# Optimization experiments

Hardware: AMD Instinct MI355X
Metric: run time of the kernel (lower is better)

The kernel has to match this reference:

```python
import jax, jax.numpy as jnp
import numpy as np

B, N, E = 32, 128, 8192
IMG, LOC, H = 2048, 5, 128


def setup_inputs() -> dict:
    key = jax.random.key(0)
    ks = jax.random.split(key, 10)
    img_feat = jax.random.normal(ks[0], (B, N, IMG), dtype=jnp.float32)
    img_loc = jax.random.uniform(ks[1], (B, N, LOC), dtype=jnp.float32)
    edge_src = jax.random.randint(ks[2], (E,), 0, N, dtype=jnp.int32)
    edge_dst = jax.random.randint(ks[3], (E,), 0, N, dtype=jnp.int32)
    # learned parameters (nn.Linear: y = x @ W + b)
    W_img = jax.random.normal(ks[4], (IMG, H), dtype=jnp.float32) / np.sqrt(IMG)
    b_img = jnp.zeros((H,), dtype=jnp.float32)
    W_loc = jax.random.normal(ks[5], (LOC, H), dtype=jnp.float32) / np.sqrt(LOC)
    b_loc = jnp.zeros((H,), dtype=jnp.float32)
    W_rel = jax.random.normal(ks[6], (2 * H, H), dtype=jnp.float32) / np.sqrt(2 * H)
    b_rel = jnp.zeros((H,), dtype=jnp.float32)
    return {
        "img_feat": img_feat, "img_loc": img_loc,
        "edge_src": edge_src, "edge_dst": edge_dst,
        "W_img": W_img, "b_img": b_img,
        "W_loc": W_loc, "b_loc": b_loc,
        "W_rel": W_rel, "b_rel": b_rel,
    }


def reference(img_feat, img_loc, edge_src, edge_dst,
              W_img, b_img, W_loc, b_loc, W_rel, b_rel):
    # img_fc / img_loc_fc projections
    img = jnp.einsum('bni,ih->bnh', img_feat, W_img) + b_img      # [B,N,H]
    loc = jnp.einsum('bnl,lh->bnh', img_loc, W_loc) + b_loc       # [B,N,H]
    node_feat = img + loc                                          # [B,N,H]
    # per-edge gather + concat + linear (batched over all edges at once;
    # split W_rel to avoid materializing the concat)
    src_f = jnp.take(img, edge_src, axis=1)                        # [B,E,H]
    dst_f = jnp.take(img, edge_dst, axis=1)                        # [B,E,H]
    edge_feat = (jnp.einsum('beh,hk->bek', src_f, W_rel[:H]) +
                 jnp.einsum('beh,hk->bek', dst_f, W_rel[H:]) + b_rel)  # [B,E,H]
    return node_feat, edge_feat
```

## Files before the change

kernel.cpp:

```cpp
#include <hip/hip_runtime.h>
#include <hip/hip_bf16.h>
#include <stdint.h>

#define B_   32
#define N_   128
#define E_   8192
#define IMG_ 2048
#define H_   128

typedef __attribute__((ext_vector_type(8))) short bf16x8;
typedef __attribute__((ext_vector_type(4))) float f32x4;

__device__ inline uint16_t f2bf(float x) {
    uint32_t u = __float_as_uint(x);
    uint32_t r = (u + 0x7FFFu + ((u >> 16) & 1u)) >> 16;
    return (uint16_t)r;
}
__device__ inline float bf2f(short x) {
    return __uint_as_float(((uint32_t)(uint16_t)x) << 16);
}

__global__ __launch_bounds__(256) void prep_kernel(
    const float* __restrict__ W_img, const float* __restrict__ W_rel,
    uint16_t* __restrict__ Wt_img, uint16_t* __restrict__ Wt_rel) {
    int bid = blockIdx.x, tid = threadIdx.x;
    if (bid < 32) {
        __shared__ float t[64][129];
        int k0 = bid * 64;
        const float* src = W_img + (size_t)k0 * H_;
        #pragma unroll
        for (int it = 0; it < 32; it++) {
            int idx = it * 256 + tid;
            t[idx >> 7][idx & 127] = src[idx];
        }
        __syncthreads();
        int c = tid >> 1, kh = (tid & 1) * 32;
        uint16_t* dst = Wt_img + (size_t)c * IMG_ + k0 + kh;
        #pragma unroll
        for (int j = 0; j < 32; j++) dst[j] = f2bf(t[kh + j][c]);
    } else {
        int t2 = (bid - 32) * 256 + tid;
        int c = t2 >> 8, k = t2 & 255;
        Wt_rel[t2] = f2bf(W_rel[k * H_ + c]);
    }
}

__global__ __launch_bounds__(1024) void node_proj_kernel(
    const float* __restrict__ img_feat,
    const uint16_t* __restrict__ Wt_img,
    const uint16_t* __restrict__ Wt_rel,
    const float* __restrict__ img_loc,
    const float* __restrict__ b_img,
    const float* __restrict__ W_loc,
    const float* __restrict__ b_loc,
    const float* __restrict__ b_rel,
    float* __restrict__ out_node,
    uint16_t* __restrict__ proj) {
    __shared__ __align__(16) char lds_raw[131072];
    float (*red)[16][128] = (float (*)[16][128])lds_raw;
    uint16_t (*imgb)[136] = (uint16_t (*)[136])lds_raw;

    int strip = blockIdx.x;
    int tid = threadIdx.x;
    int w  = tid >> 6;
    int l  = tid & 63;
    int lr = l & 15;
    int kq = l >> 4;

    const char* gA = (const char*)(img_feat + (size_t)strip * 16 * IMG_);
    #pragma unroll
    for (int r = 0; r < 8; r++) {
        int L = r * 16384 + tid * 16;
        int row = L >> 13;
        int koff = L & 8191;
        int gsrc = row * 8192 + (koff ^ ((row & 7) << 4));
        __builtin_amdgcn_global_load_lds(
            (const __attribute__((address_space(1))) void*)(gA + gsrc),
            (__attribute__((address_space(3))) void*)(lds_raw + L), 16, 0, 0);
    }

    int kbase = w * 128 + kq * 8;
    bf16x8 bcur[8];
    #pragma unroll
    for (int n = 0; n < 8; n++)
        bcur[n] = *(const bf16x8*)(Wt_img + (size_t)(n * 16 + lr) * IMG_ + kbase);

    __syncthreads();

    f32x4 acc[8];
    #pragma unroll
    for (int n = 0; n < 8; n++) acc[n] = (f32x4){0.f, 0.f, 0.f, 0.f};
    int sw = (lr & 7) << 4;
    #pragma unroll
    for (int ks = 0; ks < 4; ks++) {
        int koffb = w * 512 + ks * 128 + kq * 32;
        float4 a0 = *(const float4*)(lds_raw + (size_t)lr * 8192 + (koffb ^ sw));
        float4 a1 = *(const float4*)(lds_raw + (size_t)lr * 8192 + ((koffb + 16) ^ sw));
        bf16x8 bn[8];
        if (ks < 3) {
            int kn = kbase + (ks + 1) * 32;
            #pragma unroll
            for (int n = 0; n < 8; n++)
                bn[n] = *(const bf16x8*)(Wt_img + (size_t)(n * 16 + lr) * IMG_ + kn);
        }
        bf16x8 af;
        af[0] = (short)f2bf(a0.x); af[1] = (short)f2bf(a0.y);
        af[2] = (short)f2bf(a0.z); af[3] = (short)f2bf(a0.w);
        af[4] = (short)f2bf(a1.x); af[5] = (short)f2bf(a1.y);
        af[6] = (short)f2bf(a1.z); af[7] = (short)f2bf(a1.w);
        #pragma unroll
        for (int n = 0; n < 8; n++)
            acc[n] = __builtin_amdgcn_mfma_f32_16x16x32_bf16(af, bcur[n], acc[n], 0, 0, 0);
        if (ks < 3) {
            #pragma unroll
            for (int n = 0; n < 8; n++) bcur[n] = bn[n];
        }
    }
    __syncthreads();

    #pragma unroll
    for (int n = 0; n < 8; n++)
        #pragma unroll
        for (int r = 0; r < 4; r++)
            red[w][kq * 4 + r][n * 16 + lr] = acc[n][r];
    __syncthreads();

    int row0 = tid >> 7, col = tid & 127;
    int row1 = row0 + 8;
    float s0 = 0.f, s1 = 0.f;
    #pragma unroll
    for (int ww = 0; ww < 16; ww++) {
        s0 += red[ww][row0][col];
        s1 += red[ww][row1][col];
    }
    __syncthreads();

    {
        float bi = b_img[col];
        float bl = b_loc[col];
        float wl[5];
        #pragma unroll
        for (int j = 0; j < 5; j++) wl[j] = W_loc[j * H_ + col];
        float img0 = s0 + bi, img1 = s1 + bi;
        int g0 = strip * 16 + row0, g1 = strip * 16 + row1;
        const float* lc0 = img_loc + g0 * 5;
        const float* lc1 = img_loc + g1 * 5;
        float loc0 = bl, loc1 = bl;
        #pragma unroll
        for (int j = 0; j < 5; j++) { loc0 += lc0[j] * wl[j]; loc1 += lc1[j] * wl[j]; }
        out_node[(size_t)g0 * H_ + col] = img0 + loc0;
        out_node[(size_t)g1 * H_ + col] = img1 + loc1;
        imgb[row0][col] = f2bf(img0);
        imgb[row1][col] = f2bf(img1);
    }
    __syncthreads();

    int kl = kq * 8;
    int cp = w * 16 + lr;
    const uint16_t* bbase = (cp < 128)
        ? (Wt_rel + (size_t)cp * 256)
        : (Wt_rel + (size_t)(cp - 128) * 256 + 128);
    f32x4 pacc = (f32x4){0.f, 0.f, 0.f, 0.f};
    #pragma unroll
    for (int ks = 0; ks < 4; ks++) {
        int k = ks * 32 + kl;
        bf16x8 af = *(const bf16x8*)(&imgb[lr][k]);
        bf16x8 bf = *(const bf16x8*)(bbase + k);
        pacc = __builtin_amdgcn_mfma_f32_16x16x32_bf16(af, bf, pacc, 0, 0, 0);
    }
    float brel = (cp < 128) ? b_rel[cp] : 0.f;
    #pragma unroll
    for (int r = 0; r < 4; r++) {
        int grow = strip * 16 + kq * 4 + r;
        proj[(size_t)grow * 256 + cp] = f2bf(pacc[r] + brel);
    }
}

__global__ __launch_bounds__(256) void edge_kernel(
    const uint16_t* __restrict__ proj,
    const int* __restrict__ edge_src,
    const int* __restrict__ edge_dst,
    float* __restrict__ out_edge) {
    int t = blockIdx.x * 256 + threadIdx.x;
    #pragma unroll
    for (int it = 0; it < 8; it++) {
        int g = t + it * 524288;
        int b = g >> 17;
        int r = g & 131071;
        int e = r >> 4;
        int c = (r & 15) * 8;
        int s = edge_src[e];
        int d = edge_dst[e];
        bf16x8 a  = *(const bf16x8*)(proj + (((size_t)b * N_ + s) * 256 + c));
        bf16x8 bb = *(const bf16x8*)(proj + (((size_t)b * N_ + d) * 256 + 128 + c));
        float* op = out_edge + ((size_t)b * E_ + e) * (size_t)H_ + c;
        float4 o0, o1;
        o0.x = bf2f(a[0]) + bf2f(bb[0]);
        o0.y = bf2f(a[1]) + bf2f(bb[1]);
        o0.z = bf2f(a[2]) + bf2f(bb[2]);
        o0.w = bf2f(a[3]) + bf2f(bb[3]);
        o1.x = bf2f(a[4]) + bf2f(bb[4]);
        o1.y = bf2f(a[5]) + bf2f(bb[5]);
        o1.z = bf2f(a[6]) + bf2f(bb[6]);
        o1.w = bf2f(a[7]) + bf2f(bb[7]);
        *(float4*)op = o0;
        *(float4*)(op + 4) = o1;
    }
}

extern "C" void kernel_launch(void* const* d_in, const int* in_sizes, int n_in,
                              void* d_out, int out_size, void* d_ws, size_t ws_size,
                              hipStream_t stream) {
    const float* img_feat = (const float*)d_in[0];
    const float* img_loc  = (const float*)d_in[1];
    const int*   edge_src = (const int*)d_in[2];
    const int*   edge_dst = (const int*)d_in[3];
    const float* W_img    = (const float*)d_in[4];
    const float* b_img    = (const float*)d_in[5];
    const float* W_loc    = (const float*)d_in[6];
    const float* b_loc    = (const float*)d_in[7];
    const float* W_rel    = (const float*)d_in[8];
    const float* b_rel    = (const float*)d_in[9];

    float* out_node = (float*)d_out;
    float* out_edge = out_node + (size_t)B_ * N_ * H_;

    char* ws = (char*)d_ws;
    uint16_t* Wt_img = (uint16_t*)ws;
    uint16_t* Wt_rel = (uint16_t*)(ws + 524288);
    uint16_t* proj   = (uint16_t*)(ws + 524288 + 65536);

    prep_kernel<<<dim3(160), dim3(256), 0, stream>>>(W_img, W_rel, Wt_img, Wt_rel);

    node_proj_kernel<<<dim3(256), dim3(1024), 0, stream>>>(
        img_feat, Wt_img, Wt_rel, img_loc, b_img, W_loc, b_loc, b_rel,
        out_node, proj);

    edge_kernel<<<dim3(2048), dim3(256), 0, stream>>>(
        proj, edge_src, edge_dst, out_edge);
}
```

Measured before the change: 58.02 us.

## Fuse prep, node projection and edge gather into one kernel with flag sync

Merges the three launches into a single persistent kernel. The last 32 blocks also transpose and convert the weights, and signal readiness through a global atomic counter that all blocks spin on. Each block publishes per-batch completion flags after writing its proj rows, then runs its share of the edge gather batch by batch, waiting on those flags, and writes with nontemporal stores. This removes launch gaps and lets edge output writes overlap with the remaining projection work. In exchange it adds a memset, spin-wait latency, and a dependence on all 256 blocks being co-resident to avoid deadlock.

```diff
diff --git a/kernel.cpp b/kernel.cpp
--- a/kernel.cpp
+++ b/kernel.cpp
@@ -20,54 +20,63 @@
     return __uint_as_float(((uint32_t)(uint16_t)x) << 16);
 }
 
-__global__ __launch_bounds__(256) void prep_kernel(
-    const float* __restrict__ W_img, const float* __restrict__ W_rel,
-    uint16_t* __restrict__ Wt_img, uint16_t* __restrict__ Wt_rel) {
-    int bid = blockIdx.x, tid = threadIdx.x;
-    if (bid < 32) {
-        __shared__ float t[64][129];
-        int k0 = bid * 64;
-        const float* src = W_img + (size_t)k0 * H_;
-        #pragma unroll
-        for (int it = 0; it < 32; it++) {
-            int idx = it * 256 + tid;
-            t[idx >> 7][idx & 127] = src[idx];
-        }
-        __syncthreads();
-        int c = tid >> 1, kh = (tid & 1) * 32;
-        uint16_t* dst = Wt_img + (size_t)c * IMG_ + k0 + kh;
-        #pragma unroll
-        for (int j = 0; j < 32; j++) dst[j] = f2bf(t[kh + j][c]);
-    } else {
-        int t2 = (bid - 32) * 256 + tid;
-        int c = t2 >> 8, k = t2 & 255;
-        Wt_rel[t2] = f2bf(W_rel[k * H_ + c]);
-    }
-}
-
-__global__ __launch_bounds__(1024) void node_proj_kernel(
+__global__ __launch_bounds__(1024) void fused_kernel(
     const float* __restrict__ img_feat,
-    const uint16_t* __restrict__ Wt_img,
-    const uint16_t* __restrict__ Wt_rel,
     const float* __restrict__ img_loc,
+    const int* __restrict__ edge_src,
+    const int* __restrict__ edge_dst,
+    const float* __restrict__ W_img,
     const float* __restrict__ b_img,
     const float* __restrict__ W_loc,
     const float* __restrict__ b_loc,
+    const float* __restrict__ W_rel,
     const float* __restrict__ b_rel,
     float* __restrict__ out_node,
-    uint16_t* __restrict__ proj) {
+    float* __restrict__ out_edge,
+    uint16_t* __restrict__ Wt_img,
+    uint16_t* __restrict__ Wt_rel,
+    uint16_t* __restrict__ proj,
+    int* flags) {
     __shared__ __align__(16) char lds_raw[131072];
     float (*red)[16][128] = (float (*)[16][128])lds_raw;
     uint16_t (*imgb)[136] = (uint16_t (*)[136])lds_raw;
-
-    int strip = blockIdx.x;
+    float (*tT)[129] = (float (*)[129])lds_raw;
+
+    int bid = blockIdx.x;
     int tid = threadIdx.x;
     int w  = tid >> 6;
     int l  = tid & 63;
     int lr = l & 15;
     int kq = l >> 4;
 
-    const char* gA = (const char*)(img_feat + (size_t)strip * 16 * IMG_);
+    if (bid >= 224) {
+        int pb = bid - 224;
+        int k0 = pb * 64;
+        const float* src = W_img + (size_t)k0 * H_;
+        #pragma unroll
+        for (int it = 0; it < 8; it++) {
+            int idx = it * 1024 + tid;
+            tT[idx >> 7][idx & 127] = src[idx];
+        }
+        __syncthreads();
+        {
+            int c = tid >> 3, kh = (tid & 7) * 8;
+            uint16_t* dst = Wt_img + (size_t)c * IMG_ + k0 + kh;
+            #pragma unroll
+            for (int j = 0; j < 8; j++) dst[j] = f2bf(tT[kh + j][c]);
+        }
+        {
+            int t2 = pb * 1024 + tid;
+            int c2 = t2 >> 8, k2 = t2 & 255;
+            Wt_rel[t2] = f2bf(W_rel[k2 * H_ + c2]);
+        }
+        __syncthreads();
+        if (tid == 0)
+            __hip_atomic_fetch_add(&flags[0], 1, __ATOMIC_RELEASE,
+                                   __HIP_MEMORY_SCOPE_AGENT);
+    }
+
+    const char* gA = (const char*)(img_feat + (size_t)bid * 16 * IMG_);
     #pragma unroll
     for (int r = 0; r < 8; r++) {
         int L = r * 16384 + tid * 16;
@@ -79,13 +88,19 @@
             (__attribute__((address_space(3))) void*)(lds_raw + L), 16, 0, 0);
     }
 
+    if (tid == 0) {
+        while (__hip_atomic_load(&flags[0], __ATOMIC_RELAXED,
+                                 __HIP_MEMORY_SCOPE_AGENT) < 32) {}
+        (void)__hip_atomic_load(&flags[0], __ATOMIC_ACQUIRE,
+                                __HIP_MEMORY_SCOPE_AGENT);
+    }
+    __syncthreads();
+
     int kbase = w * 128 + kq * 8;
     bf16x8 bcur[8];
     #pragma unroll
     for (int n = 0; n < 8; n++)
         bcur[n] = *(const bf16x8*)(Wt_img + (size_t)(n * 16 + lr) * IMG_ + kbase);
-
-    __syncthreads();
 
     f32x4 acc[8];
     #pragma unroll
@@ -142,7 +157,7 @@
         #pragma unroll
         for (int j = 0; j < 5; j++) wl[j] = W_loc[j * H_ + col];
         float img0 = s0 + bi, img1 = s1 + bi;
-        int g0 = strip * 16 + row0, g1 = strip * 16 + row1;
+        int g0 = bid * 16 + row0, g1 = bid * 16 + row1;
         const float* lc0 = img_loc + g0 * 5;
         const float* lc1 = img_loc + g1 * 5;
         float loc0 = bl, loc1 = bl;
@@ -155,56 +170,65 @@
     }
     __syncthreads();
 
-    int kl = kq * 8;
-    int cp = w * 16 + lr;
-    const uint16_t* bbase = (cp < 128)
-        ? (Wt_rel + (size_t)cp * 256)
-        : (Wt_rel + (size_t)(cp - 128) * 256 + 128);
-    f32x4 pacc = (f32x4){0.f, 0.f, 0.f, 0.f};
-    #pragma unroll
-    for (int ks = 0; ks < 4; ks++) {
-        int k = ks * 32 + kl;
-        bf16x8 af = *(const bf16x8*)(&imgb[lr][k]);
-        bf16x8 bf = *(const bf16x8*)(bbase + k);
-        pacc = __builtin_amdgcn_mfma_f32_16x16x32_bf16(af, bf, pacc, 0, 0, 0);
-    }
-    float brel = (cp < 128) ? b_rel[cp] : 0.f;
-    #pragma unroll
-    for (int r = 0; r < 4; r++) {
-        int grow = strip * 16 + kq * 4 + r;
-        proj[(size_t)grow * 256 + cp] = f2bf(pacc[r] + brel);
-    }
-}
-
-__global__ __launch_bounds__(256) void edge_kernel(
-    const uint16_t* __restrict__ proj,
-    const int* __restrict__ edge_src,
-    const int* __restrict__ edge_dst,
-    float* __restrict__ out_edge) {
-    int t = blockIdx.x * 256 + threadIdx.x;
-    #pragma unroll
-    for (int it = 0; it < 8; it++) {
-        int g = t + it * 524288;
-        int b = g >> 17;
-        int r = g & 131071;
-        int e = r >> 4;
-        int c = (r & 15) * 8;
-        int s = edge_src[e];
-        int d = edge_dst[e];
-        bf16x8 a  = *(const bf16x8*)(proj + (((size_t)b * N_ + s) * 256 + c));
-        bf16x8 bb = *(const bf16x8*)(proj + (((size_t)b * N_ + d) * 256 + 128 + c));
-        float* op = out_edge + ((size_t)b * E_ + e) * (size_t)H_ + c;
-        float4 o0, o1;
-        o0.x = bf2f(a[0]) + bf2f(bb[0]);
-        o0.y = bf2f(a[1]) + bf2f(bb[1]);
-        o0.z = bf2f(a[2]) + bf2f(bb[2]);
-        o0.w = bf2f(a[3]) + bf2f(bb[3]);
-        o1.x = bf2f(a[4]) + bf2f(bb[4]);
-        o1.y = bf2f(a[5]) + bf2f(bb[5]);
-        o1.z = bf2f(a[6]) + bf2f(bb[6]);
-        o1.w = bf2f(a[7]) + bf2f(bb[7]);
-        *(float4*)op = o0;
-        *(float4*)(op + 4) = o1;
+    {
+        int kl = kq * 8;
+        int cp = w * 16 + lr;
+        const uint16_t* bbase = (cp < 128)
+            ? (Wt_rel + (size_t)cp * 256)
+            : (Wt_rel + (size_t)(cp - 128) * 256 + 128);
+        f32x4 pacc = (f32x4){0.f, 0.f, 0.f, 0.f};
+        #pragma unroll
+        for (int ks = 0; ks < 4; ks++) {
+            int k = ks * 32 + kl;
+            bf16x8 af = *(const bf16x8*)(&imgb[lr][k]);
+            bf16x8 bf = *(const bf16x8*)(bbase + k);
+            pacc = __builtin_amdgcn_mfma_f32_16x16x32_bf16(af, bf, pacc, 0, 0, 0);
+        }
+        float brel = (cp < 128) ? b_rel[cp] : 0.f;
+        #pragma unroll
+        for (int r = 0; r < 4; r++) {
+            int grow = bid * 16 + kq * 4 + r;
+            proj[(size_t)grow * 256 + cp] = f2bf(pacc[r] + brel);
+        }
+    }
+    __syncthreads();
+    if (tid == 0)
+        __hip_atomic_fetch_add(&flags[1 + (bid >> 3)], 1, __ATOMIC_RELEASE,
+                               __HIP_MEMORY_SCOPE_AGENT);
+
+    int halfsel = tid >> 9;
+    int o = (bid << 9) | (tid & 511);
+    int e = o >> 4, c = (o & 15) << 3;
+    int s = edge_src[e], d = edge_dst[e];
+    const uint16_t* ps = proj + (size_t)s * 256 + c;
+    const uint16_t* pd = proj + (size_t)d * 256 + 128 + c;
+    float* op = out_edge + (size_t)e * H_ + c;
+
+    for (int ib = 0; ib < 16; ib++) {
+        if (tid == 0) {
+            while (__hip_atomic_load(&flags[1 + 2 * ib], __ATOMIC_RELAXED,
+                                     __HIP_MEMORY_SCOPE_AGENT) < 8 ||
+                   __hip_atomic_load(&flags[2 + 2 * ib], __ATOMIC_RELAXED,
+                                     __HIP_MEMORY_SCOPE_AGENT) < 8) {}
+            (void)__hip_atomic_load(&flags[1 + 2 * ib], __ATOMIC_ACQUIRE,
+                                    __HIP_MEMORY_SCOPE_AGENT);
+        }
+        __syncthreads();
+        int b = 2 * ib + halfsel;
+        bf16x8 a  = *(const bf16x8*)(ps + (size_t)b * (N_ * 256));
+        bf16x8 bb = *(const bf16x8*)(pd + (size_t)b * (N_ * 256));
+        f32x4 o0, o1;
+        o0[0] = bf2f(a[0]) + bf2f(bb[0]);
+        o0[1] = bf2f(a[1]) + bf2f(bb[1]);
+        o0[2] = bf2f(a[2]) + bf2f(bb[2]);
+        o0[3] = bf2f(a[3]) + bf2f(bb[3]);
+        o1[0] = bf2f(a[4]) + bf2f(bb[4]);
+        o1[1] = bf2f(a[5]) + bf2f(bb[5]);
+        o1[2] = bf2f(a[6]) + bf2f(bb[6]);
+        o1[3] = bf2f(a[7]) + bf2f(bb[7]);
+        float* dst = op + (size_t)b * (E_ * H_);
+        __builtin_nontemporal_store(o0, (f32x4*)dst);
+        __builtin_nontemporal_store(o1, (f32x4*)(dst + 4));
     }
 }
 
@@ -228,14 +252,13 @@
     char* ws = (char*)d_ws;
     uint16_t* Wt_img = (uint16_t*)ws;
     uint16_t* Wt_rel = (uint16_t*)(ws + 524288);
-    uint16_t* proj   = (uint16_t*)(ws + 524288 + 65536);
-
-    prep_kernel<<<dim3(160), dim3(256), 0, stream>>>(W_img, W_rel, Wt_img, Wt_rel);
-
-    node_proj_kernel<<<dim3(256), dim3(1024), 0, stream>>>(
-        img_feat, Wt_img, Wt_rel, img_loc, b_img, W_loc, b_loc, b_rel,
-        out_node, proj);
-
-    edge_kernel<<<dim3(2048), dim3(256), 0, stream>>>(
-        proj, edge_src, edge_dst, out_edge);
-}
+    uint16_t* proj   = (uint16_t*)(ws + 589824);
+    int*      flags  = (int*)(ws + 589824 + 2097152);
+
+    (void)hipMemsetAsync(flags, 0, 256, stream);
+
+    fused_kernel<<<dim3(256), dim3(1024), 0, stream>>>(
+        img_feat, img_loc, edge_src, edge_dst,
+        W_img, b_img, W_loc, b_loc, W_rel, b_rel,
+        out_node, out_edge, Wt_img, Wt_rel, proj, flags);
+}
```

Measured after the change: 101.2 us. 1.74x slower.

## Stage per-batch projection table and edge indices in LDS for edge gather

Applied to the files above, without the earlier changes.

The edge kernel now assigns one block per (batch, 512-edge chunk). Each block loads that batch's 64KB bf16 projection table into LDS with global_load_lds and stages the edge src/dst indices in shared memory. The gathers then read from LDS instead of global/L2. This removes the repeated scattered global reads and index loads, at the cost of reloading the 64KB table once per block (16x per batch) and lower occupancy from the large LDS footprint.

```diff
diff --git a/kernel.cpp b/kernel.cpp
--- a/kernel.cpp
+++ b/kernel.cpp
@@ -176,24 +176,42 @@
     }
 }
 
-__global__ __launch_bounds__(256) void edge_kernel(
+__global__ __launch_bounds__(512) void edge_kernel(
     const uint16_t* __restrict__ proj,
     const int* __restrict__ edge_src,
     const int* __restrict__ edge_dst,
     float* __restrict__ out_edge) {
-    int t = blockIdx.x * 256 + threadIdx.x;
-    #pragma unroll
-    for (int it = 0; it < 8; it++) {
-        int g = t + it * 524288;
-        int b = g >> 17;
-        int r = g & 131071;
-        int e = r >> 4;
-        int c = (r & 15) * 8;
-        int s = edge_src[e];
-        int d = edge_dst[e];
-        bf16x8 a  = *(const bf16x8*)(proj + (((size_t)b * N_ + s) * 256 + c));
-        bf16x8 bb = *(const bf16x8*)(proj + (((size_t)b * N_ + d) * 256 + 128 + c));
-        float* op = out_edge + ((size_t)b * E_ + e) * (size_t)H_ + c;
+    __shared__ __align__(16) char plds[65536];
+    __shared__ int sidx[512];
+    __shared__ int didx[512];
+
+    int bid = blockIdx.x;
+    int b   = bid >> 4;
+    int sub = bid & 15;
+    int tid = threadIdx.x;
+
+    const char* gsrc = (const char*)(proj + (size_t)b * N_ * 256);
+    #pragma unroll
+    for (int r = 0; r < 8; r++) {
+        int L = r * 8192 + tid * 16;
+        __builtin_amdgcn_global_load_lds(
+            (const __attribute__((address_space(1))) void*)(gsrc + L),
+            (__attribute__((address_space(3))) void*)(plds + L), 16, 0, 0);
+    }
+    int e0 = sub * 512;
+    sidx[tid] = edge_src[e0 + tid];
+    didx[tid] = edge_dst[e0 + tid];
+    __syncthreads();
+
+    float* ob = out_edge + ((size_t)b * E_ + e0) * H_;
+    #pragma unroll 4
+    for (int it = 0; it < 16; it++) {
+        int i  = it * 512 + tid;
+        int el = i >> 4;
+        int c2 = (i & 15) << 4;
+        int s = sidx[el], d = didx[el];
+        bf16x8 a  = *(const bf16x8*)(plds + s * 512 + c2);
+        bf16x8 bb = *(const bf16x8*)(plds + d * 512 + 256 + c2);
         float4 o0, o1;
         o0.x = bf2f(a[0]) + bf2f(bb[0]);
         o0.y = bf2f(a[1]) + bf2f(bb[1]);
@@ -203,8 +221,9 @@
         o1.y = bf2f(a[5]) + bf2f(bb[5]);
         o1.z = bf2f(a[6]) + bf2f(bb[6]);
         o1.w = bf2f(a[7]) + bf2f(bb[7]);
-        *(float4*)op = o0;
-        *(float4*)(op + 4) = o1;
+        float* dst = ob + (size_t)i * 8;
+        *(float4*)dst = o0;
+        *(float4*)(dst + 4) = o1;
     }
 }
 
@@ -236,6 +255,6 @@
         img_feat, Wt_img, Wt_rel, img_loc, b_img, W_loc, b_loc, b_rel,
         out_node, proj);
 
-    edge_kernel<<<dim3(2048), dim3(256), 0, stream>>>(
+    edge_kernel<<<dim3(512), dim3(512), 0, stream>>>(
         proj, edge_src, edge_dst, out_edge);
 }
```

Result: slower. 60.04 us (+3.5%).
